# Performance work log

Measured on AMD Instinct MI355X. Metric: run time of the kernel, lower is better.

Reference implementation:

```python
import jax, jax.numpy as jnp
import numpy as np

S2_CH, DEM_CH, OUT_CH = 256, 64, 256
B, H, W = 4, 64, 64


def setup_inputs() -> dict:
    key = jax.random.key(0)
    ks = jax.random.split(key, 8)
    x_s2 = jax.random.normal(ks[0], (B, S2_CH, H, W), dtype=jnp.float32)
    x_dem = jax.random.normal(ks[1], (B, DEM_CH, H, W), dtype=jnp.float32)
    # 1x1 conv weights collapse to [out_ch, in_ch] matrices + bias
    Wq = jax.random.normal(ks[2], (OUT_CH, S2_CH), dtype=jnp.float32) * (S2_CH ** -0.5)
    bq = jnp.zeros((OUT_CH,), dtype=jnp.float32)
    Wk = jax.random.normal(ks[3], (OUT_CH, DEM_CH), dtype=jnp.float32) * (DEM_CH ** -0.5)
    bk = jnp.zeros((OUT_CH,), dtype=jnp.float32)
    Wv = jax.random.normal(ks[4], (OUT_CH, DEM_CH), dtype=jnp.float32) * (DEM_CH ** -0.5)
    bv = jnp.zeros((OUT_CH,), dtype=jnp.float32)
    return {"x_s2": x_s2, "x_dem": x_dem, "Wq": Wq, "bq": bq,
            "Wk": Wk, "bk": bk, "Wv": Wv, "bv": bv}


def reference(x_s2, x_dem, Wq, bq, Wk, bk, Wv, bv):
    b, c, h, w = x_s2.shape
    n = h * w
    xs = x_s2.reshape(b, c, n)                      # [b, s2_ch, n]
    xd = x_dem.reshape(b, x_dem.shape[1], n)        # [b, dem_ch, n]
    # 1x1 convs == per-pixel GEMMs
    q = jnp.einsum('oc,bcn->bon', Wq, xs) + bq[:, None]   # [b, out_ch, n]
    k = jnp.einsum('oc,bcn->bon', Wk, xd) + bk[:, None]   # [b, out_ch, n]
    v = jnp.einsum('oc,bcn->bon', Wv, xd) + bv[:, None]   # [b, out_ch, n]
    scale = q.shape[1] ** -0.5
    # attn[b,i,j] = softmax_j( k[b,:,i] . q[b,:,j] * scale )
    attn = jax.nn.softmax(jnp.einsum('bci,bcj->bij', k, q) * scale, axis=-1)
    out = jnp.einsum('bci,bij->bcj', v, attn).reshape(b, -1, h, w)
    return out + x_s2
```

## Files before the change

### kernel.cpp

```cpp
#include <hip/hip_runtime.h>
#include <hip/hip_bf16.h>
#include <cstdint>

#define B_  4
#define N_  4096
#define C_  256
#define CD_ 64

typedef unsigned short ushort_t;
typedef unsigned char uchar_t;
typedef __bf16 bf16x8 __attribute__((ext_vector_type(8)));
typedef float f32x4 __attribute__((ext_vector_type(4)));

typedef const __attribute__((address_space(1))) void* gas_t;
typedef __attribute__((address_space(3))) void* las_t;

static constexpr float SCALE_LOG2E = 0.09016844005556021f;
static constexpr float VSCALE = 8192.0f;
static constexpr float VSCALE_INV = 1.0f / 8192.0f;

__device__ __forceinline__ ushort_t f2bf(float x) {
    union { float f; unsigned u; } v; v.f = x;
    unsigned u = v.u;
    unsigned r = (u + 0x7fffu + ((u >> 16) & 1u)) >> 16;
    return (ushort_t)r;
}

__device__ __forceinline__ bf16x8 ld_bf8(const ushort_t* p) {
    return *reinterpret_cast<const bf16x8*>(p);
}

__global__ __launch_bounds__(256, 4)
void proj_q_mfma(const float* __restrict__ X, const float* __restrict__ W,
                 const float* __restrict__ bias, ushort_t* __restrict__ dst,
                 int Cin, float outScale) {
    __shared__ ushort_t sX[128][72];
    __shared__ ushort_t sW[64][72];
    const int tid = threadIdx.x;
    const int lane = tid & 63, g = lane >> 4, c16 = lane & 15;
    const int w = tid >> 6, wi = w >> 1, wj = w & 1;
    const int b = blockIdx.z, nb = blockIdx.x * 128, ob = blockIdx.y * 64;
    f32x4 acc[4][2];
#pragma unroll
    for (int nt = 0; nt < 4; ++nt)
#pragma unroll
        for (int ot = 0; ot < 2; ++ot) acc[nt][ot] = (f32x4){0.f, 0.f, 0.f, 0.f};

    const int cr = tid >> 5;
    const int n0 = (tid & 31) * 4;

    for (int k0 = 0; k0 < Cin; k0 += 64) {
#pragma unroll
        for (int p = 0; p < 8; ++p) {
            const int c = p * 8 + cr;
            float4 xv = *(const float4*)(X + ((size_t)b * Cin + k0 + c) * N_ + nb + n0);
            sX[n0 + 0][c] = f2bf(xv.x);
            sX[n0 + 1][c] = f2bf(xv.y);
            sX[n0 + 2][c] = f2bf(xv.z);
            sX[n0 + 3][c] = f2bf(xv.w);
        }
        {
            const int o = tid >> 2, cq = (tid & 3) * 16;
            const float* wsrc = W + (size_t)(ob + o) * Cin + k0 + cq;
            alignas(16) ushort_t tmp[16];
#pragma unroll
            for (int q = 0; q < 16; ++q) tmp[q] = f2bf(wsrc[q]);
            *(uint4*)&sW[o][cq]     = *(uint4*)&tmp[0];
            *(uint4*)&sW[o][cq + 8] = *(uint4*)&tmp[8];
        }
        __syncthreads();
#pragma unroll
        for (int ks = 0; ks < 2; ++ks) {
            bf16x8 af[4], bfr[2];
#pragma unroll
            for (int nt = 0; nt < 4; ++nt)
                af[nt] = *(const bf16x8*)&sX[wi * 64 + nt * 16 + c16][ks * 32 + g * 8];
#pragma unroll
            for (int ot = 0; ot < 2; ++ot)
                bfr[ot] = *(const bf16x8*)&sW[wj * 32 + ot * 16 + c16][ks * 32 + g * 8];
#pragma unroll
            for (int nt = 0; nt < 4; ++nt)
#pragma unroll
                for (int ot = 0; ot < 2; ++ot)
                    acc[nt][ot] = __builtin_amdgcn_mfma_f32_16x16x32_bf16(af[nt], bfr[ot], acc[nt][ot], 0, 0, 0);
        }
        __syncthreads();
    }
#pragma unroll
    for (int ot = 0; ot < 2; ++ot) {
        const int o = ob + wj * 32 + ot * 16 + c16;
        const float bia = bias[o];
#pragma unroll
        for (int nt = 0; nt < 4; ++nt) {
#pragma unroll
            for (int r = 0; r < 4; ++r) {
                const int n = nb + wi * 64 + nt * 16 + g * 4 + r;
                dst[((size_t)b * N_ + n) * C_ + o] = f2bf((acc[nt][ot][r] + bia) * outScale);
            }
        }
    }
}

__global__ __launch_bounds__(256, 4)
void proj_kv_mfma(const float* __restrict__ X, const float* __restrict__ Wk,
                  const float* __restrict__ bk, const float* __restrict__ Wv,
                  const float* __restrict__ bv, ushort_t* __restrict__ Kt,
                  ushort_t* __restrict__ Vm) {
    __shared__ ushort_t sX[128][72];
    __shared__ ushort_t sWk[64][72];
    __shared__ ushort_t sWv[64][72];
    const int tid = threadIdx.x;
    const int lane = tid & 63, g = lane >> 4, c16 = lane & 15;
    const int w = tid >> 6;
    const int b = blockIdx.z, nb = blockIdx.x * 128, ob = blockIdx.y * 64;

    {
        const int cr = tid >> 5, n0 = (tid & 31) * 4;
#pragma unroll
        for (int p = 0; p < 8; ++p) {
            const int c = p * 8 + cr;
            float4 xv = *(const float4*)(X + ((size_t)b * CD_ + c) * N_ + nb + n0);
            sX[n0 + 0][c] = f2bf(xv.x);
            sX[n0 + 1][c] = f2bf(xv.y);
            sX[n0 + 2][c] = f2bf(xv.z);
            sX[n0 + 3][c] = f2bf(xv.w);
        }
        const int o = tid >> 2, cq = (tid & 3) * 16;
        alignas(16) ushort_t tk[16], tv[16];
        const float* ksrc = Wk + (size_t)(ob + o) * CD_ + cq;
        const float* vsrc = Wv + (size_t)(ob + o) * CD_ + cq;
#pragma unroll
        for (int q = 0; q < 16; ++q) { tk[q] = f2bf(ksrc[q]); tv[q] = f2bf(vsrc[q]); }
        *(uint4*)&sWk[o][cq]     = *(uint4*)&tk[0];
        *(uint4*)&sWk[o][cq + 8] = *(uint4*)&tk[8];
        *(uint4*)&sWv[o][cq]     = *(uint4*)&tv[0];
        *(uint4*)&sWv[o][cq + 8] = *(uint4*)&tv[8];
    }
    __syncthreads();
    {
        const int wi = w >> 1, wj = w & 1;
        f32x4 acc[4][2];
#pragma unroll
        for (int nt = 0; nt < 4; ++nt)
#pragma unroll
            for (int ot = 0; ot < 2; ++ot) acc[nt][ot] = (f32x4){0.f, 0.f, 0.f, 0.f};
#pragma unroll
        for (int ks = 0; ks < 2; ++ks) {
            bf16x8 af[4], bfr[2];
#pragma unroll
            for (int nt = 0; nt < 4; ++nt)
                af[nt] = *(const bf16x8*)&sX[wi * 64 + nt * 16 + c16][ks * 32 + g * 8];
#pragma unroll
            for (int ot = 0; ot < 2; ++ot)
                bfr[ot] = *(const bf16x8*)&sWk[wj * 32 + ot * 16 + c16][ks * 32 + g * 8];
#pragma unroll
            for (int nt = 0; nt < 4; ++nt)
#pragma unroll
                for (int ot = 0; ot < 2; ++ot)
                    acc[nt][ot] = __builtin_amdgcn_mfma_f32_16x16x32_bf16(af[nt], bfr[ot], acc[nt][ot], 0, 0, 0);
        }
#pragma unroll
        for (int ot = 0; ot < 2; ++ot) {
            const int o = ob + wj * 32 + ot * 16 + c16;
            const float bia = bk[o];
#pragma unroll
            for (int nt = 0; nt < 4; ++nt)
#pragma unroll
                for (int r = 0; r < 4; ++r) {
                    const int n = nb + wi * 64 + nt * 16 + g * 4 + r;
                    Kt[((size_t)b * N_ + n) * C_ + o] = f2bf((acc[nt][ot][r] + bia) * SCALE_LOG2E);
                }
        }
    }
    {
        const int ow = w & 1, nw = w >> 1;
        f32x4 acc[2][4];
#pragma unroll
        for (int mt = 0; mt < 2; ++mt)
#pragma unroll
            for (int nt = 0; nt < 4; ++nt) acc[mt][nt] = (f32x4){0.f, 0.f, 0.f, 0.f};
#pragma unroll
        for (int ks = 0; ks < 2; ++ks) {
            bf16x8 af[2], bfr[4];
#pragma unroll
            for (int mt = 0; mt < 2; ++mt)
                af[mt] = *(const bf16x8*)&sWv[ow * 32 + mt * 16 + c16][ks * 32 + g * 8];
#pragma unroll
            for (int nt = 0; nt < 4; ++nt)
                bfr[nt] = *(const bf16x8*)&sX[nw * 64 + nt * 16 + c16][ks * 32 + g * 8];
#pragma unroll
            for (int mt = 0; mt < 2; ++mt)
#pragma unroll
                for (int nt = 0; nt < 4; ++nt)
                    acc[mt][nt] = __builtin_amdgcn_mfma_f32_16x16x32_bf16(af[mt], bfr[nt], acc[mt][nt], 0, 0, 0);
        }
#pragma unroll
        for (int mt = 0; mt < 2; ++mt) {
            const float4 bi4 = *(const float4*)(bv + ob + ow * 32 + mt * 16 + g * 4);
            const float bia[4] = {bi4.x, bi4.y, bi4.z, bi4.w};
#pragma unroll
            for (int nt = 0; nt < 4; ++nt) {
                const int n = nb + nw * 64 + nt * 16 + c16;
#pragma unroll
                for (int r = 0; r < 4; ++r) {
                    const int o = ob + ow * 32 + mt * 16 + g * 4 + r;
                    Vm[((size_t)b * C_ + o) * N_ + n] = f2bf(acc[mt][nt][r] + bia[r]);
                }
            }
        }
    }
}

__global__ __launch_bounds__(256, 4)
void stats_kernel(const ushort_t* __restrict__ Kt, const ushort_t* __restrict__ Qt,
                  float* __restrict__ l, uchar_t* __restrict__ PT8,
                  float* __restrict__ lpart) {
    __shared__ ushort_t smem[16384];
    uchar_t* sp8 = (uchar_t*)smem;
    float* lsum = (float*)((uchar_t*)smem + 18432);
    const int tid = threadIdx.x;
    const int lane = tid & 63, g = lane >> 4, c16 = lane & 15;
    const int w = tid >> 6, wi = w >> 1, wj = w & 1;
    const int b = blockIdx.z;
    const int ib = blockIdx.y * 128, jb = blockIdx.x * 128;
    f32x4 acc[4][4];
#pragma unroll
    for (int mt = 0; mt < 4; ++mt)
#pragma unroll
        for (int nt = 0; nt < 4; ++nt) acc[mt][nt] = (f32x4){0.f, 0.f, 0.f, 0.f};

    const int srow = tid >> 3;
    const int sc4 = tid & 7;

    for (int k0 = 0; k0 < 256; k0 += 64) {
#pragma unroll
        for (int q = 0; q < 4; ++q) {
            const int row = q * 32 + srow;
            const int gc = sc4 ^ (row & 7);
            const ushort_t* srcA = Kt + ((size_t)(b * N_ + ib + row)) * C_ + k0 + gc * 8;
            const ushort_t* srcB = Qt + ((size_t)(b * N_ + jb + row)) * C_ + k0 + gc * 8;
            __builtin_amdgcn_global_load_lds((gas_t)srcA, (las_t)&smem[(q * 256 + tid) * 8], 16, 0, 0);
            __builtin_amdgcn_global_load_lds((gas_t)srcB, (las_t)&smem[8192 + (q * 256 + tid) * 8], 16, 0, 0);
        }
        __syncthreads();
#pragma unroll
        for (int ks = 0; ks < 2; ++ks) {
            bf16x8 af[4], bf[4];
#pragma unroll
            for (int mt = 0; mt < 4; ++mt) {
                const int row = wi * 64 + mt * 16 + c16;
                af[mt] = *(const bf16x8*)&smem[row * 64 + (((ks * 4 + g) ^ (row & 7)) * 8)];
            }
#pragma unroll
            for (int nt = 0; nt < 4; ++nt) {
                const int row = wj * 64 + nt * 16 + c16;
                bf[nt] = *(const bf16x8*)&smem[8192 + row * 64 + (((ks * 4 + g) ^ (row & 7)) * 8)];
            }
#pragma unroll
            for (int mt = 0; mt < 4; ++mt)
#pragma unroll
                for (int nt = 0; nt < 4; ++nt)
                    acc[mt][nt] = __builtin_amdgcn_mfma_f32_16x16x32_bf16(af[mt], bf[nt], acc[mt][nt], 0, 0, 0);
        }
        __syncthreads();
    }
    const float sh = (PT8 != nullptr) ? 3.0f : 0.0f;
#pragma unroll
    for (int mt = 0; mt < 4; ++mt) {
        float rs[4] = {0.f, 0.f, 0.f, 0.f};
#pragma unroll
        for (int nt = 0; nt < 4; ++nt) {
            float e0 = __builtin_amdgcn_exp2f(acc[mt][nt][0] - sh);
            float e1 = __builtin_amdgcn_exp2f(acc[mt][nt][1] - sh);
            float e2 = __builtin_amdgcn_exp2f(acc[mt][nt][2] - sh);
            float e3 = __builtin_amdgcn_exp2f(acc[mt][nt][3] - sh);
            rs[0] += e0; rs[1] += e1; rs[2] += e2; rs[3] += e3;
            if (PT8 != nullptr) {
                int pk = __builtin_amdgcn_cvt_pk_fp8_f32(e0, e1, 0, false);
                pk = __builtin_amdgcn_cvt_pk_fp8_f32(e2, e3, pk, true);
                const int jl = wj * 64 + nt * 16 + c16;
                const int il = wi * 64 + mt * 16 + g * 4;
                *(int*)&sp8[jl * 144 + il] = pk;
            }
        }
#pragma unroll
        for (int r = 0; r < 4; ++r) {
            float s = rs[r];
            s += __shfl_xor(s, 1, 64);
            s += __shfl_xor(s, 2, 64);
            s += __shfl_xor(s, 4, 64);
            s += __shfl_xor(s, 8, 64);
            if (c16 == 0) {
                if (PT8 != nullptr)
                    lsum[wj * 128 + wi * 64 + mt * 16 + g * 4 + r] = s;
                else
                    atomicAdd(l + (size_t)b * N_ + ib + wi * 64 + mt * 16 + g * 4 + r, s);
            }
        }
    }
    if (PT8 != nullptr) {
        __syncthreads();
        const int chb = tid & 7;
        const int rb = tid >> 3;
#pragma unroll
        for (int r = 0; r < 4; ++r) {
            const int jl = r * 32 + rb;
            uint4 v = *(const uint4*)&sp8[jl * 144 + chb * 16];
            *(uint4*)(PT8 + ((size_t)(b * N_ + jb + jl)) * N_ + ib + chb * 16) = v;
        }
        if (tid < 128) {
            float tot = lsum[tid] + lsum[128 + tid];
            lpart[((size_t)(b * 32 + (jb >> 7))) * N_ + ib + tid] = tot;
        }
    }
}

__global__ void reduce_l_kernel(const float* __restrict__ lpart, float* __restrict__ l) {
    const int b = blockIdx.y;
    const int i = (blockIdx.x * 256 + threadIdx.x) * 4;
    float4 s = {0.f, 0.f, 0.f, 0.f};
#pragma unroll
    for (int jt = 0; jt < 32; ++jt) {
        float4 p = *(const float4*)(lpart + ((size_t)(b * 32 + jt)) * N_ + i);
        s.x += p.x; s.y += p.y; s.z += p.z; s.w += p.w;
    }
    *(float4*)(l + (size_t)b * N_ + i) = s;
}

__global__ void scale_v_kernel(const ushort_t* __restrict__ Vm, const float* __restrict__ l,
                               uchar_t* __restrict__ Vs) {
    const int i = (blockIdx.x * 256 + threadIdx.x) * 8;
    const int c = blockIdx.y, b = blockIdx.z;
    float4 l0 = *(const float4*)(l + (size_t)b * N_ + i);
    float4 l1 = *(const float4*)(l + (size_t)b * N_ + i + 4);
    float r[8] = {__builtin_amdgcn_rcpf(l0.x), __builtin_amdgcn_rcpf(l0.y),
                  __builtin_amdgcn_rcpf(l0.z), __builtin_amdgcn_rcpf(l0.w),
                  __builtin_amdgcn_rcpf(l1.x), __builtin_amdgcn_rcpf(l1.y),
                  __builtin_amdgcn_rcpf(l1.z), __builtin_amdgcn_rcpf(l1.w)};
    const size_t off = ((size_t)(b * C_ + c)) * N_ + i;
    uint4 v = *(const uint4*)(Vm + off);
    unsigned vw[4] = {v.x, v.y, v.z, v.w};
    float f[8];
#pragma unroll
    for (int q = 0; q < 4; ++q) {
        union { unsigned u; float fl; } lo, hi;
        lo.u = (vw[q] & 0xffffu) << 16;
        hi.u = vw[q] & 0xffff0000u;
        f[q * 2 + 0] = lo.fl * r[q * 2 + 0] * VSCALE;
        f[q * 2 + 1] = hi.fl * r[q * 2 + 1] * VSCALE;
    }
    int d0 = __builtin_amdgcn_cvt_pk_fp8_f32(f[0], f[1], 0, false);
    d0 = __builtin_amdgcn_cvt_pk_fp8_f32(f[2], f[3], d0, true);
    int d1 = __builtin_amdgcn_cvt_pk_fp8_f32(f[4], f[5], 0, false);
    d1 = __builtin_amdgcn_cvt_pk_fp8_f32(f[6], f[7], d1, true);
    uint2 o; o.x = (unsigned)d0; o.y = (unsigned)d1;
    *(uint2*)(Vs + off) = o;
}

__global__ __launch_bounds__(512, 4)
void gemm_out2_kernel(const uchar_t* __restrict__ A ,
                      const uchar_t* __restrict__ Bm ,
                      const float* __restrict__ R ,
                      float* __restrict__ out) {
    __shared__ uchar_t smem[73728];
    const int tid = threadIdx.x;
    const int lane = tid & 63, g = lane >> 4, c16 = lane & 15;
    const int w = tid >> 6;
    const int cw = w * 32;
    const int b = blockIdx.y;
    const int jb = blockIdx.x * 32;

    f32x4 acc[2][2];
#pragma unroll
    for (int mt = 0; mt < 2; ++mt)
#pragma unroll
        for (int nt = 0; nt < 2; ++nt) acc[mt][nt] = (f32x4){0.f, 0.f, 0.f, 0.f};

    const int sch = tid & 7;

    auto stage = [&](int k0, int dbase) {
#pragma unroll
        for (int q = 0; q < 4; ++q) {
            const int slot = q * 512 + tid;
            const int row = slot >> 3;
            const int gc = sch ^ (row & 7);
            const uchar_t* src = A + ((size_t)(b * C_ + row)) * N_ + k0 + gc * 16;
            __builtin_amdgcn_global_load_lds((gas_t)src, (las_t)&smem[dbase + slot * 16], 16, 0, 0);
        }
        if (tid < 256) {
            const int row = tid >> 3;
            const int gc = sch ^ (row & 7);
            const uchar_t* src = Bm + ((size_t)(b * N_ + jb + row)) * N_ + k0 + gc * 16;
            __builtin_amdgcn_global_load_lds((gas_t)src, (las_t)&smem[dbase + 32768 + tid * 16], 16, 0, 0);
        }
    };

    stage(0, 0);
    __syncthreads();
    for (int t = 0; t < 32; ++t) {
        const int dbase = (t & 1) * 36864;
        if (t < 31) stage((t + 1) * 128, 36864 - dbase);
        const uchar_t* sA = &smem[dbase];
        const uchar_t* sB = &smem[dbase + 32768];
#pragma unroll
        for (int ks = 0; ks < 4; ++ks) {
            const int lc = ks * 2 + (g >> 1);
            const int bo = (g & 1) * 8;
            long af[2], bfg[2];
#pragma unroll
            for (int mt = 0; mt < 2; ++mt) {
                const int row = cw + mt * 16 + c16;
                af[mt] = *(const long*)&sA[row * 128 + ((lc ^ (row & 7)) * 16) + bo];
            }
#pragma unroll
            for (int nt = 0; nt < 2; ++nt) {
                const int row = nt * 16 + c16;
                bfg[nt] = *(const long*)&sB[row * 128 + ((lc ^ (row & 7)) * 16) + bo];
            }
#pragma unroll
            for (int mt = 0; mt < 2; ++mt)
#pragma unroll
                for (int nt = 0; nt < 2; ++nt)
                    acc[mt][nt] = __builtin_amdgcn_mfma_f32_16x16x32_fp8_fp8(af[mt], bfg[nt], acc[mt][nt], 0, 0, 0);
        }
        __syncthreads();
    }
#pragma unroll
    for (int mt = 0; mt < 2; ++mt)
#pragma unroll
        for (int r = 0; r < 4; ++r) {
            const int c = cw + mt * 16 + g * 4 + r;
            const size_t rowoff = ((size_t)(b * C_ + c)) * N_ + jb;
#pragma unroll
            for (int nt = 0; nt < 2; ++nt) {
                const int j = nt * 16 + c16;
                out[rowoff + j] = R[rowoff + j] + acc[mt][nt][r] * VSCALE_INV;
            }
        }
}

__global__ __launch_bounds__(512, 4)
void out_kernel(const ushort_t* __restrict__ Kt, const ushort_t* __restrict__ Qt,
                const ushort_t* __restrict__ V, const float* __restrict__ l,
                float* __restrict__ dout) {
    __shared__ ushort_t sQ[64][264];
    __shared__ ushort_t sP[64][264];
    const int tid = threadIdx.x;
    const int w = tid >> 6, lane = tid & 63, g = lane >> 4, c16 = lane & 15;
    const int b = blockIdx.z;
    const int jb = blockIdx.x * 64;
    const int ibase = blockIdx.y * 2048;
    {
        const int jl = tid >> 3, cp = (tid & 7) * 32;
        const ushort_t* src = Qt + ((size_t)(b * N_ + jb + jl)) * C_ + cp;
        uint4 a0 = *(const uint4*)(src);
        uint4 a1 = *(const uint4*)(src + 8);
        uint4 a2 = *(const uint4*)(src + 16);
        uint4 a3 = *(const uint4*)(src + 24);
        *(uint4*)&sQ[jl][cp + 0]  = a0;
        *(uint4*)&sQ[jl][cp + 8]  = a1;
        *(uint4*)&sQ[jl][cp + 16] = a2;
        *(uint4*)&sQ[jl][cp + 24] = a3;
    }
    f32x4 acc[2][4];
#pragma unroll
    for (int mt = 0; mt < 2; ++mt)
#pragma unroll
        for (int nt = 0; nt < 4; ++nt) acc[mt][nt] = (f32x4){0.f, 0.f, 0.f, 0.f};

    const int bw = w * 32;

    for (int ic = 0; ic < 8; ++ic) {
        const int i0 = ibase + ic * 256;
        float rv[2][4];
#pragma unroll
        for (int mt = 0; mt < 2; ++mt) {
            float4 lr = *(const float4*)(l + (size_t)b * N_ + i0 + bw + mt * 16 + g * 4);
            rv[mt][0] = __builtin_amdgcn_logf(lr.x);
            rv[mt][1] = __builtin_amdgcn_logf(lr.y);
            rv[mt][2] = __builtin_amdgcn_logf(lr.z);
            rv[mt][3] = __builtin_amdgcn_logf(lr.w);
        }
        __syncthreads();
        f32x4 sa[2][4];
#pragma unroll
        for (int mt = 0; mt < 2; ++mt)
#pragma unroll
            for (int nt = 0; nt < 4; ++nt) sa[mt][nt] = (f32x4){0.f, 0.f, 0.f, 0.f};
#pragma unroll
        for (int k = 0; k < 8; ++k) {
            bf16x8 av[2];
#pragma unroll
            for (int mt = 0; mt < 2; ++mt)
                av[mt] = ld_bf8(Kt + ((size_t)(b * N_ + i0 + bw + mt * 16 + c16)) * C_ + k * 32 + g * 8);
#pragma unroll
            for (int nt = 0; nt < 4; ++nt) {
                bf16x8 bv = *(const bf16x8*)&sQ[nt * 16 + c16][k * 32 + g * 8];
#pragma unroll
                for (int mt = 0; mt < 2; ++mt)
                    sa[mt][nt] = __builtin_amdgcn_mfma_f32_16x16x32_bf16(av[mt], bv, sa[mt][nt], 0, 0, 0);
            }
        }
#pragma unroll
        for (int mt = 0; mt < 2; ++mt)
#pragma unroll
            for (int nt = 0; nt < 4; ++nt) {
                const int j = nt * 16 + c16;
                unsigned p0 = f2bf(__builtin_amdgcn_exp2f(sa[mt][nt][0] - rv[mt][0]));
                unsigned p1 = f2bf(__builtin_amdgcn_exp2f(sa[mt][nt][1] - rv[mt][1]));
                unsigned p2 = f2bf(__builtin_amdgcn_exp2f(sa[mt][nt][2] - rv[mt][2]));
                unsigned p3 = f2bf(__builtin_amdgcn_exp2f(sa[mt][nt][3] - rv[mt][3]));
                uint2 pk; pk.x = p0 | (p1 << 16); pk.y = p2 | (p3 << 16);
                *(uint2*)&sP[j][bw + mt * 16 + g * 4] = pk;
            }
        __syncthreads();
#pragma unroll
        for (int ks = 0; ks < 8; ++ks) {
            bf16x8 va[2];
#pragma unroll
            for (int mt = 0; mt < 2; ++mt)
                va[mt] = ld_bf8(V + ((size_t)(b * C_ + bw + mt * 16 + c16)) * N_ + i0 + ks * 32 + g * 8);
#pragma unroll
            for (int nt = 0; nt < 4; ++nt) {
                bf16x8 pb = *(const bf16x8*)&sP[nt * 16 + c16][ks * 32 + g * 8];
#pragma unroll
                for (int mt = 0; mt < 2; ++mt)
                    acc[mt][nt] = __builtin_amdgcn_mfma_f32_16x16x32_bf16(va[mt], pb, acc[mt][nt], 0, 0, 0);
            }
        }
    }
#pragma unroll
    for (int mt = 0; mt < 2; ++mt)
#pragma unroll
        for (int nt = 0; nt < 4; ++nt)
#pragma unroll
            for (int r = 0; r < 4; ++r) {
                const int c = bw + mt * 16 + g * 4 + r;
                const int j = jb + nt * 16 + c16;
                atomicAdd(dout + ((size_t)b * C_ + c) * N_ + j, acc[mt][nt][r]);
            }
}

extern "C" void kernel_launch(void* const* d_in, const int* in_sizes, int n_in,
                              void* d_out, int out_size, void* d_ws, size_t ws_size,
                              hipStream_t stream) {
    const float* x_s2  = (const float*)d_in[0];
    const float* x_dem = (const float*)d_in[1];
    const float* Wq = (const float*)d_in[2];
    const float* bq = (const float*)d_in[3];
    const float* Wk = (const float*)d_in[4];
    const float* bk = (const float*)d_in[5];
    const float* Wv = (const float*)d_in[6];
    const float* bv = (const float*)d_in[7];
    float* out = (float*)d_out;

    const size_t MiB = 1024 * 1024;
    char* ws = (char*)d_ws;
    ushort_t* Qt = (ushort_t*)(ws);
    ushort_t* Kt = (ushort_t*)(ws + 8  * MiB);
    ushort_t* Vm = (ushort_t*)(ws + 16 * MiB);
    uchar_t*  Vs = (uchar_t*) (ws + 24 * MiB);
    float*    lp = (float*)   (ws + 24 * MiB);
    float*    lv = (float*)   (ws + 28 * MiB);
    uchar_t*  PT = (uchar_t*) (ws + 29 * MiB);
    const bool bigws = ws_size >= 93 * MiB;

    if (!bigws) {
        hipMemsetAsync(lv, 0, (size_t)B_ * N_ * sizeof(float), stream);
        hipMemcpyAsync(out, x_s2, (size_t)B_ * C_ * N_ * sizeof(float),
                       hipMemcpyDeviceToDevice, stream);
    }

    proj_q_mfma<<<dim3(N_ / 128, C_ / 64, B_), 256, 0, stream>>>(x_s2, Wq, bq, Qt, C_, 1.0f);
    proj_kv_mfma<<<dim3(N_ / 128, C_ / 64, B_), 256, 0, stream>>>(x_dem, Wk, bk, Wv, bv, Kt, Vm);
    stats_kernel<<<dim3(N_ / 128, N_ / 128, B_), 256, 0, stream>>>(Kt, Qt, lv,
                                                                   bigws ? PT : (uchar_t*)nullptr,
                                                                   lp);
    if (bigws) {
        reduce_l_kernel<<<dim3(N_ / 1024, B_), 256, 0, stream>>>(lp, lv);
        scale_v_kernel<<<dim3(N_ / 2048, C_, B_), 256, 0, stream>>>(Vm, lv, Vs);
        gemm_out2_kernel<<<dim3(N_ / 32, B_), 512, 0, stream>>>(Vs, PT, x_s2, out);
    } else {
        out_kernel<<<dim3(N_ / 64, 2, B_), 512, 0, stream>>>(Kt, Qt, Vm, lv, out);
    }
}
```

Baseline: 208.3 us.

## Double-buffer stats kernel K/Q staging and use nontemporal stores for outputs

The stats kernel's K/Q tile staging is reworked from four 64-wide k-chunks with a single buffer into eight 32-wide chunks ping-ponged between two LDS buffers. The next chunk's global-to-LDS load is issued before computing on the current one, so load latency can overlap with MFMA work, and the XOR swizzle is adjusted for the new row width. Separately, the FP8 probability writes and the residual read and output write in the PV kernel now use nontemporal loads and stores to reduce cache pollution. Shrinking each k-step to 32 elements halves MFMA work per barrier, which adds synchronisation overhead.

```diff
diff --git a/kernel.cpp b/kernel.cpp
--- a/kernel.cpp
+++ b/kernel.cpp
@@ -11,6 +11,7 @@
 typedef unsigned char uchar_t;
 typedef __bf16 bf16x8 __attribute__((ext_vector_type(8)));
 typedef float f32x4 __attribute__((ext_vector_type(4)));
+typedef unsigned int u32x4 __attribute__((ext_vector_type(4)));
 
 typedef const __attribute__((address_space(1))) void* gas_t;
 typedef __attribute__((address_space(3))) void* las_t;
@@ -216,8 +217,9 @@
                   float* __restrict__ l, uchar_t* __restrict__ PT8,
                   float* __restrict__ lpart) {
     __shared__ ushort_t smem[16384];
-    uchar_t* sp8 = (uchar_t*)smem;
-    float* lsum = (float*)((uchar_t*)smem + 18432);
+    uchar_t* smem8 = (uchar_t*)smem;
+    uchar_t* sp8 = smem8;
+    float* lsum = (float*)(smem8 + 18432);
     const int tid = threadIdx.x;
     const int lane = tid & 63, g = lane >> 4, c16 = lane & 15;
     const int w = tid >> 6, wi = w >> 1, wj = w & 1;
@@ -229,39 +231,42 @@
 #pragma unroll
         for (int nt = 0; nt < 4; ++nt) acc[mt][nt] = (f32x4){0.f, 0.f, 0.f, 0.f};
 
-    const int srow = tid >> 3;
-    const int sc4 = tid & 7;
-
-    for (int k0 = 0; k0 < 256; k0 += 64) {
-#pragma unroll
-        for (int q = 0; q < 4; ++q) {
-            const int row = q * 32 + srow;
-            const int gc = sc4 ^ (row & 7);
-            const ushort_t* srcA = Kt + ((size_t)(b * N_ + ib + row)) * C_ + k0 + gc * 8;
-            const ushort_t* srcB = Qt + ((size_t)(b * N_ + jb + row)) * C_ + k0 + gc * 8;
-            __builtin_amdgcn_global_load_lds((gas_t)srcA, (las_t)&smem[(q * 256 + tid) * 8], 16, 0, 0);
-            __builtin_amdgcn_global_load_lds((gas_t)srcB, (las_t)&smem[8192 + (q * 256 + tid) * 8], 16, 0, 0);
-        }
-        __syncthreads();
-#pragma unroll
-        for (int ks = 0; ks < 2; ++ks) {
-            bf16x8 af[4], bf[4];
-#pragma unroll
-            for (int mt = 0; mt < 4; ++mt) {
-                const int row = wi * 64 + mt * 16 + c16;
-                af[mt] = *(const bf16x8*)&smem[row * 64 + (((ks * 4 + g) ^ (row & 7)) * 8)];
-            }
-#pragma unroll
-            for (int nt = 0; nt < 4; ++nt) {
-                const int row = wj * 64 + nt * 16 + c16;
-                bf[nt] = *(const bf16x8*)&smem[8192 + row * 64 + (((ks * 4 + g) ^ (row & 7)) * 8)];
-            }
-#pragma unroll
-            for (int mt = 0; mt < 4; ++mt)
-#pragma unroll
-                for (int nt = 0; nt < 4; ++nt)
-                    acc[mt][nt] = __builtin_amdgcn_mfma_f32_16x16x32_bf16(af[mt], bf[nt], acc[mt][nt], 0, 0, 0);
-        }
+    const int srow = tid >> 2;
+    const int sc = tid & 3;
+
+    auto stage = [&](int kc, int dbase) {
+#pragma unroll
+        for (int q = 0; q < 2; ++q) {
+            const int row = q * 64 + srow;
+            const int gc = sc ^ ((row >> 1) & 3);
+            const ushort_t* srcA = Kt + ((size_t)(b * N_ + ib + row)) * C_ + kc * 32 + gc * 8;
+            const ushort_t* srcB = Qt + ((size_t)(b * N_ + jb + row)) * C_ + kc * 32 + gc * 8;
+            __builtin_amdgcn_global_load_lds((gas_t)srcA, (las_t)&smem8[dbase + (q * 256 + tid) * 16], 16, 0, 0);
+            __builtin_amdgcn_global_load_lds((gas_t)srcB, (las_t)&smem8[dbase + 8192 + (q * 256 + tid) * 16], 16, 0, 0);
+        }
+    };
+
+    stage(0, 0);
+    __syncthreads();
+    for (int t = 0; t < 8; ++t) {
+        const int dbase = (t & 1) * 16384;
+        if (t < 7) stage(t + 1, 16384 - dbase);
+        bf16x8 af[4], bf[4];
+#pragma unroll
+        for (int mt = 0; mt < 4; ++mt) {
+            const int row = wi * 64 + mt * 16 + c16;
+            af[mt] = *(const bf16x8*)&smem8[dbase + row * 64 + ((g ^ ((row >> 1) & 3)) * 16)];
+        }
+#pragma unroll
+        for (int nt = 0; nt < 4; ++nt) {
+            const int row = wj * 64 + nt * 16 + c16;
+            bf[nt] = *(const bf16x8*)&smem8[dbase + 8192 + row * 64 + ((g ^ ((row >> 1) & 3)) * 16)];
+        }
+#pragma unroll
+        for (int mt = 0; mt < 4; ++mt)
+#pragma unroll
+            for (int nt = 0; nt < 4; ++nt)
+                acc[mt][nt] = __builtin_amdgcn_mfma_f32_16x16x32_bf16(af[mt], bf[nt], acc[mt][nt], 0, 0, 0);
         __syncthreads();
     }
     const float sh = (PT8 != nullptr) ? 3.0f : 0.0f;
@@ -305,8 +310,9 @@
 #pragma unroll
         for (int r = 0; r < 4; ++r) {
             const int jl = r * 32 + rb;
-            uint4 v = *(const uint4*)&sp8[jl * 144 + chb * 16];
-            *(uint4*)(PT8 + ((size_t)(b * N_ + jb + jl)) * N_ + ib + chb * 16) = v;
+            u32x4 v = *(const u32x4*)&sp8[jl * 144 + chb * 16];
+            __builtin_nontemporal_store(v,
+                (u32x4*)(PT8 + ((size_t)(b * N_ + jb + jl)) * N_ + ib + chb * 16));
         }
         if (tid < 128) {
             float tot = lsum[tid] + lsum[128 + tid];
@@ -434,7 +440,9 @@
 #pragma unroll
             for (int nt = 0; nt < 2; ++nt) {
                 const int j = nt * 16 + c16;
-                out[rowoff + j] = R[rowoff + j] + acc[mt][nt][r] * VSCALE_INV;
+                float rv = __builtin_nontemporal_load(&R[rowoff + j]);
+                __builtin_nontemporal_store(rv + acc[mt][nt][r] * VSCALE_INV,
+                                            &out[rowoff + j]);
             }
         }
 }
```

Result: no change. 204.9 us (-1.6%).
